# Optimization experiments

Measured on AMD Instinct MI355X. Metric: run time of the kernel, lower is better.

## Reference

```python
import jax, jax.numpy as jnp
import numpy as np

N = 100000
E = 1600000
M_NNZ = 800000
C_IN = 64
C_OUT = 64
D = 64
N_MOTIF = 13


def setup_inputs() -> dict:
    key = jax.random.key(0)
    ks = jax.random.split(key, 12)
    x = jax.random.normal(ks[0], (N, C_IN), dtype=jnp.float32)
    edge_index = jax.random.randint(ks[1], (2, E), 0, N, dtype=jnp.int32)
    edge_weight = jax.random.uniform(ks[2], (E,), dtype=jnp.float32)
    motif_src = jax.random.randint(ks[3], (N_MOTIF, M_NNZ), 0, N, dtype=jnp.int32)
    motif_dst = jax.random.randint(ks[4], (N_MOTIF, M_NNZ), 0, N, dtype=jnp.int32)
    motif_val = jax.random.uniform(ks[5], (N_MOTIF, M_NNZ), dtype=jnp.float32)
    scale = 0.05
    W_rel = jax.random.normal(ks[6], (C_IN, C_OUT), dtype=jnp.float32) * scale
    root = jax.random.normal(ks[7], (C_IN, C_OUT), dtype=jnp.float32) * scale
    bias = jnp.zeros((C_OUT,), dtype=jnp.float32)
    wa = jax.random.normal(ks[8], (C_OUT, D), dtype=jnp.float32) * scale
    ba = jnp.zeros((D,), dtype=jnp.float32)
    motif_W = jax.random.normal(ks[9], (N_MOTIF, C_OUT * 13, D), dtype=jnp.float32) * scale
    motif_b = jnp.zeros((N_MOTIF, D), dtype=jnp.float32)
    return {
        'x': x, 'edge_index': edge_index, 'edge_weight': edge_weight,
        'motif_src': motif_src, 'motif_dst': motif_dst, 'motif_val': motif_val,
        'W_rel': W_rel, 'root': root, 'bias': bias,
        'wa': wa, 'ba': ba, 'motif_W': motif_W, 'motif_b': motif_b,
    }


def reference(x, edge_index, edge_weight, motif_src, motif_dst, motif_val,
              W_rel, root, bias, wa, ba, motif_W, motif_b):
    n = x.shape[0]
    src, dst = edge_index[0], edge_index[1]

    # GCNConv(normalize=False, bias=False): h[dst] += w_e * (x @ W)[src]
    xw = x @ W_rel
    h = jax.ops.segment_sum(edge_weight[:, None] * xw[src], dst, num_segments=n)

    # aggr == 'mean': divide by in-degree (1/deg, inf -> 0)
    degs = jax.ops.segment_sum(jnp.ones_like(edge_weight), dst, num_segments=n)
    norm = jnp.where(degs > 0, 1.0 / degs, 0.0)
    h = h * norm[:, None]

    # root weight + bias
    h = h + x @ root + bias

    # 13 sparse motif aggregations: motif_rsts[i+1] = motif_mats[i] @ h
    motif_rsts = [h]
    for i in range(N_MOTIF):
        agg = jax.ops.segment_sum(motif_val[i][:, None] * h[motif_src[i]],
                                  motif_dst[i], num_segments=n)
        motif_rsts.append(agg)

    # per-motif attention-weighted compression (eval mode -> dropouts are identity)
    motif_embeds = []
    for i in range(1, N_MOTIF + 1):
        compress = jnp.concatenate(motif_rsts[:i] + motif_rsts[i + 1:], axis=1)  # [N, 13*C]
        mw = motif_rsts[i] @ wa + ba                       # [N, D]
        c = compress @ motif_W[i - 1] + motif_b[i - 1]     # [N, D]
        att = jax.nn.sigmoid(jnp.sum(mw * c, axis=1, keepdims=True))  # [N, 1]
        motif_embeds.append(att * (mw - c))
    return jnp.concatenate(motif_embeds, axis=1)  # [N, 13*D]
```

## Files before the change

kernel.cpp:

```cpp
#include <hip/hip_runtime.h>
#include <math.h>

#define NN 100000
#define NE 1600000
#define MNZ 800000
#define NM 13
#define SLICE_W 12500

typedef __attribute__((ext_vector_type(8))) short short8;
typedef __attribute__((ext_vector_type(4))) float floatx4;

__device__ __forceinline__ unsigned short f2bf(float f) {
    unsigned int u = __float_as_uint(f);
    u += 0x7FFFu + ((u >> 16) & 1u);
    return (unsigned short)(u >> 16);
}

__global__ __launch_bounds__(256) void k_xw(const float* __restrict__ x,
                                            const float* __restrict__ W,
                                            float* __restrict__ out) {
    __shared__ float Wl[64 * 64];
    __shared__ float xl[4][64];
    int t = threadIdx.x;
    for (int s = t; s < 4096; s += 256) Wl[s] = W[s];
    int nl = t >> 6, d = t & 63;
    int n = blockIdx.x * 4 + nl;
    xl[nl][d] = x[n * 64 + d];
    __syncthreads();
    float acc = 0.f;
#pragma unroll
    for (int k = 0; k < 64; ++k) acc = fmaf(xl[nl][k], Wl[k * 64 + d], acc);
    out[n * 64 + d] = acc;
}

__global__ __launch_bounds__(256) void k_hist_m(const int* __restrict__ mdst,
                                                int* __restrict__ cnt) {
    int m = blockIdx.y;
    int j = blockIdx.x * 256 + threadIdx.x;
    int d = mdst[(long long)m * MNZ + j];
    atomicAdd(&cnt[m * NN + d], 1);
}

__global__ __launch_bounds__(256) void k_hist_e(const int* __restrict__ ei,
                                                int* __restrict__ cnt) {
    int e = blockIdx.x * 256 + threadIdx.x;
    atomicAdd(&cnt[ei[NE + e]], 1);
}

__global__ __launch_bounds__(256) void k_alloc(const int* __restrict__ cnt,
                                               int* __restrict__ off,
                                               int* __restrict__ fill,
                                               int* __restrict__ cursor, int n) {
    __shared__ int sc[256];
    __shared__ int sbase;
    int m = blockIdx.y;
    int t = threadIdx.x;
    int d = blockIdx.x * 256 + t;
    int c = (d < n) ? cnt[(long long)m * n + d] : 0;
    sc[t] = c;
    __syncthreads();
    for (int s = 1; s < 256; s <<= 1) {
        int add = (t >= s) ? sc[t - s] : 0;
        __syncthreads();
        sc[t] += add;
        __syncthreads();
    }
    int incl = sc[t];
    int excl = incl - c;
    if (t == 255) sbase = atomicAdd(cursor + m, incl);
    __syncthreads();
    if (d < n) {
        int o = sbase + excl;
        off[(long long)m * n + d] = o;
        fill[(long long)m * n + d] = o;
    }
}

__global__ __launch_bounds__(256) void k_scat_m(const int* __restrict__ msrc,
                                                const int* __restrict__ mdst,
                                                const float* __restrict__ mval,
                                                int* __restrict__ fill,
                                                int2* __restrict__ sm) {
    int m = blockIdx.y;
    int slice = blockIdx.x & 7;
    long long idx = (long long)m * MNZ + (long long)(blockIdx.x >> 3) * 256 + threadIdx.x;
    int d = mdst[idx];
    if (d / SLICE_W == slice) {
        int p = atomicAdd(&fill[m * NN + d], 1);
        sm[(long long)m * MNZ + p] = make_int2(msrc[idx], __float_as_int(mval[idx]));
    }
}

__global__ __launch_bounds__(256) void k_scat_e(const int* __restrict__ ei,
                                                const float* __restrict__ ew,
                                                int* __restrict__ fill,
                                                int2* __restrict__ se) {
    int slice = blockIdx.x & 7;
    int e = (blockIdx.x >> 3) * 256 + threadIdx.x;
    int d = ei[NE + e];
    if (d / SLICE_W == slice) {
        int p = atomicAdd(&fill[d], 1);
        se[p] = make_int2(ei[e], __float_as_int(ew[e]));
    }
}

__global__ __launch_bounds__(256) void k_gath_e(const int2* __restrict__ se,
                                                const int* __restrict__ off,
                                                const int* __restrict__ cnt,
                                                const float* __restrict__ XW,
                                                float* __restrict__ H) {
    int sub = threadIdx.x >> 4, l = threadIdx.x & 15;
    int d = blockIdx.x * 16 + sub;
    int o = off[d], c = cnt[d];
    const int2* ep = se + o;
    floatx4 acc = (floatx4)0.f;
    int e = 0;
    for (; e + 1 < c; e += 2) {
        int2 a = ep[e], b = ep[e + 1];
        floatx4 ha = *(const floatx4*)&XW[(long long)a.x * 64 + l * 4];
        floatx4 hb = *(const floatx4*)&XW[(long long)b.x * 64 + l * 4];
        float va = __int_as_float(a.y), vb = __int_as_float(b.y);
#pragma unroll
        for (int q = 0; q < 4; ++q) acc[q] = fmaf(va, ha[q], acc[q]);
#pragma unroll
        for (int q = 0; q < 4; ++q) acc[q] = fmaf(vb, hb[q], acc[q]);
    }
    if (e < c) {
        int2 a = ep[e];
        floatx4 ha = *(const floatx4*)&XW[(long long)a.x * 64 + l * 4];
        float va = __int_as_float(a.y);
#pragma unroll
        for (int q = 0; q < 4; ++q) acc[q] = fmaf(va, ha[q], acc[q]);
    }
    *(floatx4*)&H[(long long)d * 64 + l * 4] = acc;
}

__global__ __launch_bounds__(256) void k_fin(const float* __restrict__ x,
                                             const float* __restrict__ root,
                                             const float* __restrict__ bias,
                                             const int* __restrict__ cnt_e,
                                             float* __restrict__ H,
                                             unsigned short* __restrict__ Rb) {
    __shared__ float Wl[64 * 64];
    __shared__ float xl[4][64];
    int t = threadIdx.x;
    for (int s = t; s < 4096; s += 256) Wl[s] = root[s];
    int nl = t >> 6, d = t & 63;
    int n = blockIdx.x * 4 + nl;
    xl[nl][d] = x[n * 64 + d];
    __syncthreads();
    float acc = 0.f;
#pragma unroll
    for (int k = 0; k < 64; ++k) acc = fmaf(xl[nl][k], Wl[k * 64 + d], acc);
    int dg = cnt_e[n];
    float nm = dg > 0 ? 1.0f / (float)dg : 0.f;
    long long idx = (long long)n * 64 + d;
    float hv = H[idx] * nm + acc + bias[d];
    H[idx] = hv;
    Rb[idx] = f2bf(hv);
}

__global__ __launch_bounds__(256) void k_gath_m(const int2* __restrict__ sm,
                                                const int* __restrict__ off,
                                                const int* __restrict__ cnt,
                                                const float* __restrict__ H,
                                                unsigned short* __restrict__ Rb) {
    int m = blockIdx.y;
    int sub = threadIdx.x >> 4, l = threadIdx.x & 15;
    int d = blockIdx.x * 16 + sub;
    long long mi = (long long)m * NN + d;
    int o = off[mi], c = cnt[mi];
    const int2* ep = sm + (long long)m * MNZ + o;
    floatx4 acc = (floatx4)0.f;
    int e = 0;
    for (; e + 1 < c; e += 2) {
        int2 a = ep[e], b = ep[e + 1];
        floatx4 ha = *(const floatx4*)&H[(long long)a.x * 64 + l * 4];
        floatx4 hb = *(const floatx4*)&H[(long long)b.x * 64 + l * 4];
        float va = __int_as_float(a.y), vb = __int_as_float(b.y);
#pragma unroll
        for (int q = 0; q < 4; ++q) acc[q] = fmaf(va, ha[q], acc[q]);
#pragma unroll
        for (int q = 0; q < 4; ++q) acc[q] = fmaf(vb, hb[q], acc[q]);
    }
    if (e < c) {
        int2 a = ep[e];
        floatx4 ha = *(const floatx4*)&H[(long long)a.x * 64 + l * 4];
        float va = __int_as_float(a.y);
#pragma unroll
        for (int q = 0; q < 4; ++q) acc[q] = fmaf(va, ha[q], acc[q]);
    }
    unsigned int lo = (unsigned int)f2bf(acc[0]) | ((unsigned int)f2bf(acc[1]) << 16);
    unsigned int hi = (unsigned int)f2bf(acc[2]) | ((unsigned int)f2bf(acc[3]) << 16);
    *(uint2*)&Rb[((long long)(m + 1) * NN + d) * 64 + l * 4] = make_uint2(lo, hi);
}

__global__ void k_wt(const float* __restrict__ mW, unsigned short* __restrict__ WT) {
    int n = blockIdx.y;
    int k = blockIdx.x * 128 + threadIdx.x;
    int i = (n >> 6) + 1;
    int d = n & 63;
    int r = k >> 6;
    int kk = k & 63;
    float v = 0.f;
    if (r != i) {
        int j = (r < i) ? r : r - 1;
        v = mW[((long long)(i - 1) * 832 + (j * 64 + kk)) * 64 + d];
    }
    WT[(long long)n * 896 + k] = f2bf(v);
}

#define BM 128
#define LDA 72

__global__ __launch_bounds__(256) void k_gemm(const unsigned short* __restrict__ Rb,
                                              const unsigned short* __restrict__ WT,
                                              const float* __restrict__ wa,
                                              const float* __restrict__ ba,
                                              const float* __restrict__ mb,
                                              float* __restrict__ out) {
    int im1 = blockIdx.x;
    int i = im1 + 1;
    int row0 = blockIdx.y * BM;
    int t = threadIdx.x;
    int w = t >> 6;
    int lane = t & 63;
    int quad = lane >> 4;
    int l16 = lane & 15;

    __shared__ __align__(16) unsigned short Al[BM * LDA];
    __shared__ __align__(16) unsigned short Bl[64 * LDA];
    __shared__ __align__(16) unsigned short waTl[64 * LDA];

    for (int s = t; s < 4096; s += 256) {
        int k = s >> 6, d = s & 63;
        waTl[d * LDA + k] = f2bf(wa[s]);
    }

    floatx4 acc[2][4];
    floatx4 mwa[2][4];
#pragma unroll
    for (int a = 0; a < 2; ++a)
#pragma unroll
        for (int b = 0; b < 4; ++b) { acc[a][b] = (floatx4)0.f; mwa[a][b] = (floatx4)0.f; }

    for (int kb = 0; kb < 15; ++kb) {
        int kchunk = (kb < 14) ? kb : i;
        __syncthreads();
#pragma unroll
        for (int s = 0; s < 4; ++s) {
            int lin = t + s * 256;
            int rr = lin >> 3;
            int k8 = (lin & 7) * 8;
            int grow = row0 + rr;
            short8 v = (short8)0;
            if (grow < NN) v = *(const short8*)&Rb[((long long)kchunk * NN + grow) * 64 + k8];
            *(short8*)&Al[rr * LDA + k8] = v;
        }
        if (kb < 14) {
#pragma unroll
            for (int s = 0; s < 4; ++s) {
                int lin4 = t + s * 256;
                int n = lin4 >> 4;
                int k4 = (lin4 & 15) * 4;
                const unsigned short* src = &WT[(long long)(im1 * 64 + n) * 896 + kb * 64 + k4];
                *(unsigned long long*)&Bl[n * LDA + k4] = *(const unsigned long long*)src;
            }
        }
        __syncthreads();
#pragma unroll
        for (int kk = 0; kk < 64; kk += 32) {
            short8 af[2];
#pragma unroll
            for (int mt = 0; mt < 2; ++mt)
                af[mt] = *(const short8*)&Al[((w * 2 + mt) * 16 + l16) * LDA + kk + quad * 8];
            if (kb < 14) {
#pragma unroll
                for (int nt = 0; nt < 4; ++nt) {
                    short8 bf = *(const short8*)&Bl[(nt * 16 + l16) * LDA + kk + quad * 8];
#pragma unroll
                    for (int mt = 0; mt < 2; ++mt)
                        acc[mt][nt] = __builtin_amdgcn_mfma_f32_16x16x32_bf16(af[mt], bf, acc[mt][nt], 0, 0, 0);
                }
            } else {
#pragma unroll
                for (int nt = 0; nt < 4; ++nt) {
                    short8 bf = *(const short8*)&waTl[(nt * 16 + l16) * LDA + kk + quad * 8];
#pragma unroll
                    for (int mt = 0; mt < 2; ++mt)
                        mwa[mt][nt] = __builtin_amdgcn_mfma_f32_16x16x32_bf16(af[mt], bf, mwa[mt][nt], 0, 0, 0);
                }
            }
        }
    }

#pragma unroll
    for (int mt = 0; mt < 2; ++mt) {
        float cv[4][4], mv[4][4];
#pragma unroll
        for (int nt = 0; nt < 4; ++nt) {
            int col = nt * 16 + l16;
            float mbv = mb[im1 * 64 + col];
            float bav = ba[col];
#pragma unroll
            for (int r = 0; r < 4; ++r) {
                cv[nt][r] = acc[mt][nt][r] + mbv;
                mv[nt][r] = mwa[mt][nt][r] + bav;
            }
        }
        int grow_base = row0 + (w * 2 + mt) * 16 + quad * 4;
#pragma unroll
        for (int r = 0; r < 4; ++r) {
            float s = 0.f;
#pragma unroll
            for (int nt = 0; nt < 4; ++nt) s += mv[nt][r] * cv[nt][r];
            s += __shfl_xor(s, 1);
            s += __shfl_xor(s, 2);
            s += __shfl_xor(s, 4);
            s += __shfl_xor(s, 8);
            float att = 1.f / (1.f + __expf(-s));
            int grow = grow_base + r;
            if (grow < NN) {
#pragma unroll
                for (int nt = 0; nt < 4; ++nt)
                    out[(long long)grow * 832 + im1 * 64 + nt * 16 + l16] = att * (mv[nt][r] - cv[nt][r]);
            }
        }
    }
}

extern "C" void kernel_launch(void* const* d_in, const int* in_sizes, int n_in,
                              void* d_out, int out_size, void* d_ws, size_t ws_size,
                              hipStream_t stream) {
    const float* x    = (const float*)d_in[0];
    const int*   ei   = (const int*)d_in[1];
    const float* ew   = (const float*)d_in[2];
    const int*   msrc = (const int*)d_in[3];
    const int*   mdst = (const int*)d_in[4];
    const float* mval = (const float*)d_in[5];
    const float* Wrel = (const float*)d_in[6];
    const float* root = (const float*)d_in[7];
    const float* bias = (const float*)d_in[8];
    const float* wa   = (const float*)d_in[9];
    const float* ba   = (const float*)d_in[10];
    const float* mW   = (const float*)d_in[11];
    const float* mb   = (const float*)d_in[12];
    float* out = (float*)d_out;

    unsigned short* Rb = (unsigned short*)d_ws;
    float* H  = (float*)(Rb + (size_t)14 * NN * 64);
    float* XW = H + (size_t)NN * 64;
    unsigned short* WT = (unsigned short*)(XW + (size_t)NN * 64);
    int2* sm = (int2*)(WT + (size_t)832 * 896);
    int2* se = sm + (size_t)NM * MNZ;
    int* cnt_m  = (int*)(se + NE);
    int* cnt_e  = cnt_m + (size_t)NM * NN;
    int* cursors = cnt_e + NN;
    int* off_m  = cursors + 16;
    int* fill_m = off_m + (size_t)NM * NN;
    int* off_e  = fill_m + (size_t)NM * NN;
    int* fill_e = off_e + NN;

    hipMemsetAsync(cnt_m, 0, sizeof(int) * ((size_t)NM * NN + NN + 16), stream);

    k_xw<<<NN / 4, 256, 0, stream>>>(x, Wrel, XW);
    k_hist_m<<<dim3(MNZ / 256, NM), 256, 0, stream>>>(mdst, cnt_m);
    k_hist_e<<<NE / 256, 256, 0, stream>>>(ei, cnt_e);
    k_alloc<<<dim3((NN + 255) / 256, NM), 256, 0, stream>>>(cnt_m, off_m, fill_m, cursors, NN);
    k_alloc<<<dim3((NN + 255) / 256, 1), 256, 0, stream>>>(cnt_e, off_e, fill_e, cursors + NM, NN);
    k_scat_m<<<dim3((MNZ / 256) * 8, NM), 256, 0, stream>>>(msrc, mdst, mval, fill_m, sm);
    k_scat_e<<<(NE / 256) * 8, 256, 0, stream>>>(ei, ew, fill_e, se);
    k_gath_e<<<NN / 16, 256, 0, stream>>>(se, off_e, cnt_e, XW, H);
    k_fin<<<NN / 4, 256, 0, stream>>>(x, root, bias, cnt_e, H, Rb);
    k_gath_m<<<dim3(NN / 16, NM), 256, 0, stream>>>(sm, off_m, cnt_m, H, Rb);
    k_wt<<<dim3(7, 832), 128, 0, stream>>>(mW, WT);
    k_gemm<<<dim3(NM, (NN + BM - 1) / BM), 256, 0, stream>>>(Rb, WT, wa, ba, mb, out);
}
```

Before: 2.454 ms.

## Swizzle GEMM LDS layout, remap blocks per XCD, reuse B tile for wa

Replaces the padded LDS layout (LDA 72) with an XOR-swizzled 64-wide layout for the A and B tiles, avoiding bank conflicts without padding. The B tile now loads with 16-byte vectors. The separate waT shared buffer is removed, and wa is written into the B buffer on the final k-step, which cuts LDS usage and may allow more resident workgroups. The 2D grid becomes a 1D grid with an XCD-aware remap, so the 13 motif blocks of a row tile land on the same XCD and share the Rb chunks in L2.

```diff
diff --git a/kernel.cpp b/kernel.cpp
--- a/kernel.cpp
+++ b/kernel.cpp
@@ -211,7 +211,8 @@
 }
 
 #define BM 128
-#define LDA 72
+#define NTY ((NN + BM - 1) / BM)
+#define GEMM_NWG (NM * NTY)
 
 __global__ __launch_bounds__(256) void k_gemm(const unsigned short* __restrict__ Rb,
                                               const unsigned short* __restrict__ WT,
@@ -219,23 +220,22 @@
                                               const float* __restrict__ ba,
                                               const float* __restrict__ mb,
                                               float* __restrict__ out) {
-    int im1 = blockIdx.x;
+    const int nwg = GEMM_NWG, q = nwg >> 3, r = nwg & 7;
+    int lin = blockIdx.x;
+    int xcd = lin & 7, pos = lin >> 3;
+    int v = (xcd < r ? xcd * (q + 1) : r * (q + 1) + (xcd - r) * q) + pos;
+    int row_t = v / NM;
+    int im1 = v - row_t * NM;
     int i = im1 + 1;
-    int row0 = blockIdx.y * BM;
+    int row0 = row_t * BM;
     int t = threadIdx.x;
     int w = t >> 6;
     int lane = t & 63;
     int quad = lane >> 4;
     int l16 = lane & 15;
 
-    __shared__ __align__(16) unsigned short Al[BM * LDA];
-    __shared__ __align__(16) unsigned short Bl[64 * LDA];
-    __shared__ __align__(16) unsigned short waTl[64 * LDA];
-
-    for (int s = t; s < 4096; s += 256) {
-        int k = s >> 6, d = s & 63;
-        waTl[d * LDA + k] = f2bf(wa[s]);
-    }
+    __shared__ __align__(16) unsigned short Al[BM * 64];
+    __shared__ __align__(16) unsigned short Bl[64 * 64];
 
     floatx4 acc[2][4];
     floatx4 mwa[2][4];
@@ -249,43 +249,48 @@
         __syncthreads();
 #pragma unroll
         for (int s = 0; s < 4; ++s) {
-            int lin = t + s * 256;
-            int rr = lin >> 3;
-            int k8 = (lin & 7) * 8;
+            int lin8 = t + s * 256;
+            int rr = lin8 >> 3;
+            int g = lin8 & 7;
             int grow = row0 + rr;
-            short8 v = (short8)0;
-            if (grow < NN) v = *(const short8*)&Rb[((long long)kchunk * NN + grow) * 64 + k8];
-            *(short8*)&Al[rr * LDA + k8] = v;
+            short8 vv = (short8)0;
+            if (grow < NN) vv = *(const short8*)&Rb[((long long)kchunk * NN + grow) * 64 + g * 8];
+            *(short8*)&Al[rr * 64 + ((g ^ (rr & 7)) << 3)] = vv;
         }
         if (kb < 14) {
 #pragma unroll
-            for (int s = 0; s < 4; ++s) {
-                int lin4 = t + s * 256;
-                int n = lin4 >> 4;
-                int k4 = (lin4 & 15) * 4;
-                const unsigned short* src = &WT[(long long)(im1 * 64 + n) * 896 + kb * 64 + k4];
-                *(unsigned long long*)&Bl[n * LDA + k4] = *(const unsigned long long*)src;
+            for (int s = 0; s < 2; ++s) {
+                int lin8 = t + s * 256;
+                int n = lin8 >> 3;
+                int g = lin8 & 7;
+                short8 vv = *(const short8*)&WT[(long long)(im1 * 64 + n) * 896 + kb * 64 + g * 8];
+                *(short8*)&Bl[n * 64 + ((g ^ (n & 7)) << 3)] = vv;
+            }
+        } else {
+            for (int s = t; s < 4096; s += 256) {
+                int k = s >> 6, d = s & 63;
+                Bl[d * 64 + (((k >> 3) ^ (d & 7)) << 3) + (k & 7)] = f2bf(wa[s]);
             }
         }
         __syncthreads();
 #pragma unroll
         for (int kk = 0; kk < 64; kk += 32) {
+            int g0 = (kk >> 3) + quad;
             short8 af[2];
 #pragma unroll
-            for (int mt = 0; mt < 2; ++mt)
-                af[mt] = *(const short8*)&Al[((w * 2 + mt) * 16 + l16) * LDA + kk + quad * 8];
-            if (kb < 14) {
-#pragma unroll
-                for (int nt = 0; nt < 4; ++nt) {
-                    short8 bf = *(const short8*)&Bl[(nt * 16 + l16) * LDA + kk + quad * 8];
+            for (int mt = 0; mt < 2; ++mt) {
+                int arow = (w * 2 + mt) * 16 + l16;
+                af[mt] = *(const short8*)&Al[arow * 64 + ((g0 ^ (arow & 7)) << 3)];
+            }
+#pragma unroll
+            for (int nt = 0; nt < 4; ++nt) {
+                int brow = nt * 16 + l16;
+                short8 bf = *(const short8*)&Bl[brow * 64 + ((g0 ^ (brow & 7)) << 3)];
+                if (kb < 14) {
 #pragma unroll
                     for (int mt = 0; mt < 2; ++mt)
                         acc[mt][nt] = __builtin_amdgcn_mfma_f32_16x16x32_bf16(af[mt], bf, acc[mt][nt], 0, 0, 0);
-                }
-            } else {
-#pragma unroll
-                for (int nt = 0; nt < 4; ++nt) {
-                    short8 bf = *(const short8*)&waTl[(nt * 16 + l16) * LDA + kk + quad * 8];
+                } else {
 #pragma unroll
                     for (int mt = 0; mt < 2; ++mt)
                         mwa[mt][nt] = __builtin_amdgcn_mfma_f32_16x16x32_bf16(af[mt], bf, mwa[mt][nt], 0, 0, 0);
@@ -303,27 +308,27 @@
             float mbv = mb[im1 * 64 + col];
             float bav = ba[col];
 #pragma unroll
-            for (int r = 0; r < 4; ++r) {
-                cv[nt][r] = acc[mt][nt][r] + mbv;
-                mv[nt][r] = mwa[mt][nt][r] + bav;
+            for (int r2 = 0; r2 < 4; ++r2) {
+                cv[nt][r2] = acc[mt][nt][r2] + mbv;
+                mv[nt][r2] = mwa[mt][nt][r2] + bav;
             }
         }
         int grow_base = row0 + (w * 2 + mt) * 16 + quad * 4;
 #pragma unroll
-        for (int r = 0; r < 4; ++r) {
+        for (int r2 = 0; r2 < 4; ++r2) {
             float s = 0.f;
 #pragma unroll
-            for (int nt = 0; nt < 4; ++nt) s += mv[nt][r] * cv[nt][r];
+            for (int nt = 0; nt < 4; ++nt) s += mv[nt][r2] * cv[nt][r2];
             s += __shfl_xor(s, 1);
             s += __shfl_xor(s, 2);
             s += __shfl_xor(s, 4);
             s += __shfl_xor(s, 8);
             float att = 1.f / (1.f + __expf(-s));
-            int grow = grow_base + r;
+            int grow = grow_base + r2;
             if (grow < NN) {
 #pragma unroll
                 for (int nt = 0; nt < 4; ++nt)
-                    out[(long long)grow * 832 + im1 * 64 + nt * 16 + l16] = att * (mv[nt][r] - cv[nt][r]);
+                    out[(long long)grow * 832 + im1 * 64 + nt * 16 + l16] = att * (mv[nt][r2] - cv[nt][r2]);
             }
         }
     }
@@ -374,5 +379,5 @@
     k_fin<<<NN / 4, 256, 0, stream>>>(x, root, bias, cnt_e, H, Rb);
     k_gath_m<<<dim3(NN / 16, NM), 256, 0, stream>>>(sm, off_m, cnt_m, H, Rb);
     k_wt<<<dim3(7, 832), 128, 0, stream>>>(mW, WT);
-    k_gemm<<<dim3(NM, (NN + BM - 1) / BM), 256, 0, stream>>>(Rb, WT, wa, ba, mb, out);
-}
+    k_gemm<<<GEMM_NWG, 256, 0, stream>>>(Rb, WT, wa, ba, mb, out);
+}
```

Result: slower. 2.609 ms (+6.3%).
